# Optimization experiments

Measured on AMD Instinct MI355X. Metric: run time of the kernel, lower is better.

Reference implementation:

```python
import jax, jax.numpy as jnp
import numpy as np

B, T, C = 8, 2048, 1024
E = 8            # num_experts (= world_size in the original)
K = 2            # top-k
CAP_FACTOR = 1.25
CAPACITY = int(T / E * CAP_FACTOR)  # 320, per (expert, batch-row)
DFF = 4 * C


def setup_inputs() -> dict:
    key = jax.random.key(0)
    ks = jax.random.split(key, 4)
    x = jax.random.normal(ks[0], (B, T, C), dtype=jnp.float32)
    Wg = jax.random.normal(ks[1], (C, E), dtype=jnp.float32) * (C ** -0.5)
    bg = jnp.zeros((E,), dtype=jnp.float32)
    W1 = jax.random.normal(ks[2], (E, C, DFF), dtype=jnp.float32) * (C ** -0.5)
    b1 = jnp.zeros((E, DFF), dtype=jnp.float32)
    W2 = jax.random.normal(ks[3], (E, DFF, C), dtype=jnp.float32) * (DFF ** -0.5)
    b2 = jnp.zeros((E, C), dtype=jnp.float32)
    return {"x": x, "Wg": Wg, "bg": bg, "W1": W1, "b1": b1, "W2": W2, "b2": b2}


def reference(x, Wg, bg, W1, b1, W2, b2):
    # Router: linear + softmax, then top-k gating
    probs = jax.nn.softmax(jnp.einsum('btc,ce->bte', x, Wg) + bg, axis=-1)  # [B,T,E]
    topk_p, topk_e = jax.lax.top_k(probs, K)                               # [B,T,K]

    S = T * K  # one "assignment" per (token, k-slot), row-major (t, k) order
    e_flat = topk_e.reshape(B, S)                      # expert id per assignment
    p_flat = topk_p.reshape(B, S)

    # Position of each assignment within its (batch-row, expert) group,
    # ordered by token position then k-slot (matches nonzero() row-major order).
    onehot = (e_flat[..., None] == jnp.arange(E)).astype(jnp.int32)        # [B,S,E]
    pos_all = jnp.cumsum(onehot, axis=1) - 1                                # [B,S,E]
    pos = jnp.take_along_axis(pos_all, e_flat[..., None], axis=2)[..., 0]   # [B,S]
    keep = pos < CAPACITY                               # overflow tokens are dropped

    # Dispatch tokens into padded per-(expert,row) buffers: [E,B,CAPACITY,C]
    x_rep = jnp.repeat(x, K, axis=1)                    # [B,S,C], assignment order
    b_idx = jnp.broadcast_to(jnp.arange(B)[:, None], (B, S))
    pos_scat = jnp.where(keep, pos, CAPACITY)           # out-of-range -> dropped
    dispatch = jnp.zeros((E, B, CAPACITY, C), dtype=x.dtype)
    dispatch = dispatch.at[e_flat, b_idx, pos_scat].set(x_rep, mode='drop')

    # Grouped expert FFN (padding rows are zeros; their outputs are never read back)
    h = jax.nn.relu(jnp.einsum('ebsc,ech->ebsh', dispatch, W1) + b1[:, None, None, :])
    y = jnp.einsum('ebsh,ehc->ebsc', h, W2) + b2[:, None, None, :]

    # Combine: gather back, scale by gate prob (dropped tokens -> padding_val 0)
    gathered = y[e_flat, b_idx, jnp.clip(pos, 0, CAPACITY - 1)]             # [B,S,C]
    out = gathered * jnp.where(keep, p_flat, 0.0)[..., None]
    return out.reshape(B, T, K, C).sum(axis=2)          # sum over k assignments
```

## Files before the change

kernel.cpp:

```cpp
#include <hip/hip_runtime.h>
#include <stdint.h>

#define B_ 8
#define T_ 2048
#define C_ 1024
#define E_ 8
#define K_ 2
#define CAP_ 320
#define DFF_ 4096
#define S_ (T_*K_)
#define NTOK (B_*T_)
#define ROWS_PER_E (B_*CAP_)

typedef __attribute__((ext_vector_type(8))) short short8;
typedef __attribute__((ext_vector_type(4))) float floatx4;

__device__ __forceinline__ unsigned short f2bf(float f) {
  union { float f; unsigned u; } v; v.f = f;
  unsigned r = v.u + 0x7fffu + ((v.u >> 16) & 1u);
  return (unsigned short)(r >> 16);
}
__device__ __forceinline__ float bf2f(unsigned short h) {
  union { unsigned u; float f; } v; v.u = ((unsigned)h) << 16;
  return v.f;
}

#define GLOAD16(g, l) __builtin_amdgcn_global_load_lds( \
    (const __attribute__((address_space(1))) void*)(g), \
    (__attribute__((address_space(3))) void*)(l), 16, 0, 0)

__global__ void router_kernel(const float* __restrict__ x, const float* __restrict__ Wg,
                              const float* __restrict__ bg,
                              int* __restrict__ topk_e, float* __restrict__ topk_p)
{
  int token = (int)((blockIdx.x * blockDim.x + threadIdx.x) >> 6);
  int lane = threadIdx.x & 63;
  if (token >= NTOK) return;
  const float* xr = x + (size_t)token * C_;
  double acc[E_];
  #pragma unroll
  for (int e = 0; e < E_; ++e) acc[e] = 0.0;
  for (int c = lane; c < C_; c += 64) {
    double xv = (double)xr[c];
    const float4* w4 = (const float4*)(Wg + (size_t)c * E_);
    float4 wa = w4[0], wb = w4[1];
    acc[0] += xv * (double)wa.x; acc[1] += xv * (double)wa.y;
    acc[2] += xv * (double)wa.z; acc[3] += xv * (double)wa.w;
    acc[4] += xv * (double)wb.x; acc[5] += xv * (double)wb.y;
    acc[6] += xv * (double)wb.z; acc[7] += xv * (double)wb.w;
  }
  #pragma unroll
  for (int off = 32; off; off >>= 1) {
    #pragma unroll
    for (int e = 0; e < E_; ++e) acc[e] += __shfl_down(acc[e], off, 64);
  }
  if (lane == 0) {
    double lg[E_];
    double mx = -1e300;
    #pragma unroll
    for (int e = 0; e < E_; ++e) { lg[e] = acc[e] + (double)bg[e]; mx = fmax(mx, lg[e]); }
    double se = 0.0, pr[E_];
    #pragma unroll
    for (int e = 0; e < E_; ++e) { pr[e] = exp(lg[e] - mx); se += pr[e]; }
    #pragma unroll
    for (int e = 0; e < E_; ++e) pr[e] /= se;
    int e0 = 0;
    #pragma unroll
    for (int e = 1; e < E_; ++e) if (pr[e] > pr[e0]) e0 = e;
    int e1 = -1;
    #pragma unroll
    for (int e = 0; e < E_; ++e) {
      if (e == e0) continue;
      if (e1 < 0 || pr[e] > pr[e1]) e1 = e;
    }
    topk_e[token*2+0] = e0; topk_p[token*2+0] = (float)pr[e0];
    topk_e[token*2+1] = e1; topk_p[token*2+1] = (float)pr[e1];
  }
}

__global__ void scan_kernel(const int* __restrict__ topk_e,
                            int* __restrict__ pos_arr,
                            int* __restrict__ slot_src,
                            int* __restrict__ counts)
{
  const int b = blockIdx.x;
  const int tid = threadIdx.x;
  const int PT = S_ / 256;
  __shared__ int cnt[256][E_];
  int e_loc[16];
  int local[E_];
  #pragma unroll
  for (int e = 0; e < E_; ++e) local[e] = 0;
  const int* te = topk_e + (size_t)b * S_;
  for (int j = 0; j < PT; ++j) {
    int e = te[tid*PT + j];
    e_loc[j] = e;
    local[e]++;
  }
  #pragma unroll
  for (int e = 0; e < E_; ++e) cnt[tid][e] = local[e];
  __syncthreads();
  if (tid < E_) {
    int run = 0;
    for (int i = 0; i < 256; ++i) { int v = cnt[i][tid]; cnt[i][tid] = run; run += v; }
    counts[tid*B_ + b] = run;
  }
  __syncthreads();
  int base[E_];
  #pragma unroll
  for (int e = 0; e < E_; ++e) base[e] = cnt[tid][e];
  for (int j = 0; j < PT; ++j) {
    int e = e_loc[j];
    int p = base[e]++;
    int s = tid*PT + j;
    if (p < CAP_) {
      pos_arr[(size_t)b*S_ + s] = p;
      slot_src[((size_t)e*B_ + b)*CAP_ + p] = s >> 1;
    } else {
      pos_arr[(size_t)b*S_ + s] = -1;
    }
  }
}

__global__ void transpose_conv_kernel(const float* __restrict__ in, unsigned short* __restrict__ out,
                                      int R, int Cc)
{
  __shared__ float tile[32][33];
  const int e = blockIdx.z;
  const float* ine = in + (size_t)e * R * Cc;
  unsigned short* oute = out + (size_t)e * R * Cc;
  const int c0 = blockIdx.x * 32, r0 = blockIdx.y * 32;
  const int tx = threadIdx.x & 7, ty = threadIdx.x >> 3;
  float4 v = *(const float4*)(ine + (size_t)(r0 + ty) * Cc + c0 + tx*4);
  tile[ty][tx*4+0] = v.x; tile[ty][tx*4+1] = v.y;
  tile[ty][tx*4+2] = v.z; tile[ty][tx*4+3] = v.w;
  __syncthreads();
  ushort4 o;
  o.x = f2bf(tile[tx*4+0][ty]);
  o.y = f2bf(tile[tx*4+1][ty]);
  o.z = f2bf(tile[tx*4+2][ty]);
  o.w = f2bf(tile[tx*4+3][ty]);
  *(ushort4*)(oute + (size_t)(c0 + ty) * R + r0 + tx*4) = o;
}

__global__ void dispatch_kernel(const float* __restrict__ x, const int* __restrict__ slot_src,
                                const int* __restrict__ counts, unsigned short* __restrict__ Xd,
                                int e_base, int nexp)
{
  int row = (int)((blockIdx.x * blockDim.x + threadIdx.x) >> 6);
  int lane = threadIdx.x & 63;
  int total = nexp * B_ * CAP_;
  if (row >= total) return;
  int el = row / (B_*CAP_);
  int rem = row - el*(B_*CAP_);
  int b = rem / CAP_, slot = rem - b*CAP_;
  int eg = e_base + el;
  int cnt = counts[eg*B_ + b]; if (cnt > CAP_) cnt = CAP_;
  unsigned short* orow = Xd + (size_t)row * C_;
  if (slot < cnt) {
    int t = slot_src[((size_t)eg*B_ + b)*CAP_ + slot];
    const float4* xr = (const float4*)(x + ((size_t)b*T_ + t)*C_);
    #pragma unroll
    for (int i = 0; i < C_/256; ++i) {
      float4 v = xr[i*64 + lane];
      ushort4 o;
      o.x = f2bf(v.x); o.y = f2bf(v.y); o.z = f2bf(v.z); o.w = f2bf(v.w);
      ((ushort4*)orow)[i*64 + lane] = o;
    }
  } else {
    ushort4 z; z.x = z.y = z.z = z.w = 0;
    #pragma unroll
    for (int i = 0; i < C_/256; ++i) ((ushort4*)orow)[i*64 + lane] = z;
  }
}

template<int RELU>
__global__ __launch_bounds__(512) void gemm256_kernel(
    const unsigned short* __restrict__ A,
    const unsigned short* __restrict__ BT,
    const float* __restrict__ bias,
    unsigned short* __restrict__ Out0,
    unsigned short* __restrict__ Out1,
    int M, int N, int Kfull, int klen, int tilesPerSplit, int nwg)
{
  __shared__ __align__(16) unsigned short lds[4*16384];
  const int NT = N >> 8, MT = M >> 8;
  const int bid = blockIdx.x;
  const int wg = (bid & 7) * (nwg >> 3) + (bid >> 3);
  const int sp  = wg / tilesPerSplit;
  const int wgr = wg - sp * tilesPerSplit;
  const int e  = wgr / (MT*NT);
  const int r2 = wgr - e*(MT*NT);
  const int mt = r2 / NT, nt = r2 - mt*NT;
  const int k0 = sp * klen;
  const unsigned short* Ae = A + (size_t)e * M * Kfull;
  const unsigned short* Be = BT + (size_t)e * N * Kfull;
  const float* be = bias ? (bias + (size_t)e * N) : nullptr;
  unsigned short* Oe = (sp == 0 ? Out0 : Out1) + (size_t)e * M * N;
  const int m0 = mt*256, n0 = nt*256;

  const int tid = threadIdx.x, lane = tid & 63, w = tid >> 6;
  const int wr = w >> 2, wc = w & 3;

  floatx4 acc[8][4];
  #pragma unroll
  for (int i = 0; i < 8; ++i)
    #pragma unroll
    for (int j = 0; j < 4; ++j) acc[i][j] = (floatx4){0.f, 0.f, 0.f, 0.f};

  const int c0 = tid, c1 = 512 + tid;
  const int sr0 = c0 >> 2, sr1 = c1 >> 2;
  const int sq0 = ((c0 & 3) * 8) ^ (((sr0 >> 1) & 3) << 3);
  const int sq1 = ((c1 & 3) * 8) ^ (((sr1 >> 1) & 3) << 3);
  const unsigned short* gA0 = Ae + (size_t)(m0 + sr0)*Kfull + k0 + sq0;
  const unsigned short* gA1 = Ae + (size_t)(m0 + sr1)*Kfull + k0 + sq1;
  const unsigned short* gB0 = Be + (size_t)(n0 + sr0)*Kfull + k0 + sq0;
  const unsigned short* gB1 = Be + (size_t)(n0 + sr1)*Kfull + k0 + sq1;
  const int ldsOff0 = w*512;
  const int ldsOff1 = 4096 + w*512;

  const int fr = lane & 15, kq = lane >> 4;
  const int aRow = wr*128 + fr;
  const int bRow = wc*64 + fr;
  const int aOff = aRow*32 + ((kq*8) ^ (((aRow >> 1) & 3) << 3));
  const int bOff = 8192 + bRow*32 + ((kq*8) ^ (((bRow >> 1) & 3) << 3));

  const int nk = klen >> 5;

#define STAGE_A(t, slot) do { \
    GLOAD16(gA0 + (size_t)(t)*32, lds + (slot)*16384 + ldsOff0); \
    GLOAD16(gA1 + (size_t)(t)*32, lds + (slot)*16384 + ldsOff1); } while(0)
#define STAGE_B(t, slot) do { \
    GLOAD16(gB0 + (size_t)(t)*32, lds + (slot)*16384 + 8192 + ldsOff0); \
    GLOAD16(gB1 + (size_t)(t)*32, lds + (slot)*16384 + 8192 + ldsOff1); } while(0)

  STAGE_A(0, 0); STAGE_B(0, 0);
  STAGE_A(1, 1); STAGE_B(1, 1);
  STAGE_A(2, 2); STAGE_B(2, 2);
  asm volatile("s_waitcnt vmcnt(8)" ::: "memory");
  __builtin_amdgcn_s_barrier();

  for (int t = 0; t < nk; ++t) {
    const int slot = t & 3, ps = (t + 3) & 3;
    const unsigned short* sT = lds + slot*16384;
    const bool pf = (t + 3 < nk);
    short8 bfr[4], afLo[4], afHi[4];

    #pragma unroll
    for (int nf = 0; nf < 4; ++nf) bfr[nf] = *(const short8*)(sT + bOff + nf*512);
    #pragma unroll
    for (int mf = 0; mf < 4; ++mf) afLo[mf] = *(const short8*)(sT + aOff + mf*512);
    __builtin_amdgcn_sched_barrier(0);
    #pragma unroll
    for (int mf = 0; mf < 4; ++mf) afHi[mf] = *(const short8*)(sT + aOff + (mf+4)*512);
    if (pf) { STAGE_A(t+3, ps); STAGE_B(t+3, ps); }
    asm volatile("s_waitcnt lgkmcnt(4)" ::: "memory");
    __builtin_amdgcn_sched_barrier(0);
    __builtin_amdgcn_s_setprio(1);
    #pragma unroll
    for (int mf = 0; mf < 4; ++mf)
      #pragma unroll
      for (int nf = 0; nf < 4; ++nf)
        acc[mf][nf] = __builtin_amdgcn_mfma_f32_16x16x32_bf16(afLo[mf], bfr[nf], acc[mf][nf], 0, 0, 0);
    __builtin_amdgcn_s_setprio(0);
    __builtin_amdgcn_sched_barrier(0);
    asm volatile("s_waitcnt lgkmcnt(0)" ::: "memory");
    __builtin_amdgcn_sched_barrier(0);
    __builtin_amdgcn_s_setprio(1);
    #pragma unroll
    for (int mf = 0; mf < 4; ++mf)
      #pragma unroll
      for (int nf = 0; nf < 4; ++nf)
        acc[mf+4][nf] = __builtin_amdgcn_mfma_f32_16x16x32_bf16(afHi[mf], bfr[nf], acc[mf+4][nf], 0, 0, 0);
    __builtin_amdgcn_s_setprio(0);
    __builtin_amdgcn_sched_barrier(0);

    if (t + 1 < nk) {
      if (t + 3 < nk)      asm volatile("s_waitcnt vmcnt(8)" ::: "memory");
      else if (t + 2 < nk) asm volatile("s_waitcnt vmcnt(4)" ::: "memory");
      else                 asm volatile("s_waitcnt vmcnt(0)" ::: "memory");
      __builtin_amdgcn_s_barrier();
    }
  }
#undef STAGE_A
#undef STAGE_B

  const int col = lane & 15, rbase = (lane >> 4) * 4;
  #pragma unroll
  for (int mf = 0; mf < 8; ++mf) {
    const int gr0 = m0 + wr*128 + mf*16 + rbase;
    #pragma unroll
    for (int nf = 0; nf < 4; ++nf) {
      const int gc = n0 + wc*64 + nf*16 + col;
      const float bv = be ? be[gc] : 0.f;
      #pragma unroll
      for (int r = 0; r < 4; ++r) {
        float v = acc[mf][nf][r] + bv;
        if (RELU) v = fmaxf(v, 0.f);
        Oe[(size_t)(gr0 + r)*N + gc] = f2bf(v);
      }
    }
  }
}

__global__ void combine_kernel(const unsigned short* __restrict__ Y0,
                               const unsigned short* __restrict__ Y1,
                               const float* __restrict__ b2c,
                               const int* __restrict__ topk_e, const float* __restrict__ topk_p,
                               const int* __restrict__ pos_arr, float* __restrict__ out)
{
  int token = (int)((blockIdx.x * blockDim.x + threadIdx.x) >> 6);
  int lane = threadIdx.x & 63;
  if (token >= NTOK) return;
  int b = token / T_, t = token - b*T_;
  int s0 = b*S_ + t*2;
  float acc[16];
  #pragma unroll
  for (int i = 0; i < 16; ++i) acc[i] = 0.f;
  #pragma unroll
  for (int k = 0; k < 2; ++k) {
    int pos = pos_arr[s0 + k];
    if (pos < 0) continue;
    int e = topk_e[s0 + k];
    float p = topk_p[s0 + k];
    size_t rowoff = (((size_t)e*B_ + b)*CAP_ + pos) * C_;
    const unsigned short* yr0 = Y0 + rowoff;
    const unsigned short* yr1 = Y1 ? (Y1 + rowoff) : nullptr;
    const float* bb = b2c ? (b2c + (size_t)e * C_) : nullptr;
    #pragma unroll
    for (int i = 0; i < 4; ++i) {
      ushort4 v = ((const ushort4*)yr0)[i*64 + lane];
      float s0v = bf2f(v.x), s1v = bf2f(v.y), s2v = bf2f(v.z), s3v = bf2f(v.w);
      if (yr1) {
        ushort4 u = ((const ushort4*)yr1)[i*64 + lane];
        s0v += bf2f(u.x); s1v += bf2f(u.y); s2v += bf2f(u.z); s3v += bf2f(u.w);
      }
      if (bb) {
        float4 bv = ((const float4*)bb)[i*64 + lane];
        s0v += bv.x; s1v += bv.y; s2v += bv.z; s3v += bv.w;
      }
      acc[i*4+0] += p * s0v;
      acc[i*4+1] += p * s1v;
      acc[i*4+2] += p * s2v;
      acc[i*4+3] += p * s3v;
    }
  }
  float4* orow = (float4*)(out + (size_t)token * C_);
  #pragma unroll
  for (int i = 0; i < 4; ++i) {
    float4 o;
    o.x = acc[i*4+0]; o.y = acc[i*4+1]; o.z = acc[i*4+2]; o.w = acc[i*4+3];
    orow[i*64 + lane] = o;
  }
}

extern "C" void kernel_launch(void* const* d_in, const int* in_sizes, int n_in,
                              void* d_out, int out_size, void* d_ws, size_t ws_size,
                              hipStream_t stream)
{
  const float* x  = (const float*)d_in[0];
  const float* Wg = (const float*)d_in[1];
  const float* bg = (const float*)d_in[2];
  const float* W1 = (const float*)d_in[3];
  const float* b1 = (const float*)d_in[4];
  const float* W2 = (const float*)d_in[5];
  const float* b2 = (const float*)d_in[6];
  float* out = (float*)d_out;

  char* ws = (char*)d_ws;
  size_t off = 0;
  auto alloc = [&](size_t bytes) -> char* {
    char* p = ws + off;
    off = (off + bytes + 255) & ~(size_t)255;
    return p;
  };
  int*   topk_e  = (int*)  alloc((size_t)NTOK * K_ * 4);
  float* topk_p  = (float*)alloc((size_t)NTOK * K_ * 4);
  int*   pos_arr = (int*)  alloc((size_t)B_ * S_ * 4);
  int*   slot_src= (int*)  alloc((size_t)E_ * B_ * CAP_ * 4);
  int*   counts  = (int*)  alloc((size_t)E_ * B_ * 4);
  unsigned short* Ybuf = (unsigned short*)alloc((size_t)E_ * ROWS_PER_E * C_ * 2);
  size_t fixed = off;
  const size_t perE = (size_t)C_ * DFF_ * 2
                    + (size_t)ROWS_PER_E * C_ * 2
                    + (size_t)ROWS_PER_E * DFF_ * 2
                    + 3 * 256;
  int k = 8;
  while (k > 1 && fixed + (size_t)k * perE > ws_size) k >>= 1;
  unsigned short* Wt = (unsigned short*)alloc((size_t)k * C_ * DFF_ * 2);
  unsigned short* Xd = (unsigned short*)alloc((size_t)k * ROWS_PER_E * C_ * 2);
  unsigned short* Hb = (unsigned short*)alloc((size_t)k * ROWS_PER_E * DFF_ * 2);

  router_kernel<<<NTOK/4, 256, 0, stream>>>(x, Wg, bg, topk_e, topk_p);
  scan_kernel<<<B_, 256, 0, stream>>>(topk_e, pos_arr, slot_src, counts);

  const bool splitK2 = (k == 8);

  for (int eb = 0; eb < E_; eb += k) {
    transpose_conv_kernel<<<dim3(DFF_/32, C_/32, k), 256, 0, stream>>>(
        W1 + (size_t)eb * C_ * DFF_, Wt, C_, DFF_);
    dispatch_kernel<<<(k * ROWS_PER_E) / 4, 256, 0, stream>>>(x, slot_src, counts, Xd, eb, k);
    {
      int tiles = k * (ROWS_PER_E/256) * (DFF_/256);
      gemm256_kernel<1><<<tiles, 512, 0, stream>>>(
          Xd, Wt, b1 + (size_t)eb * DFF_, Hb, Hb, ROWS_PER_E, DFF_, C_, C_, tiles, tiles);
    }
    transpose_conv_kernel<<<dim3(C_/32, DFF_/32, k), 256, 0, stream>>>(
        W2 + (size_t)eb * DFF_ * C_, Wt, DFF_, C_);
    {
      int tiles = k * (ROWS_PER_E/256) * (C_/256);
      if (splitK2) {
        gemm256_kernel<0><<<2*tiles, 512, 0, stream>>>(
            Hb, Wt, nullptr, Ybuf, Xd, ROWS_PER_E, C_, DFF_, DFF_/2, tiles, 2*tiles);
      } else {
        gemm256_kernel<0><<<tiles, 512, 0, stream>>>(
            Hb, Wt, b2 + (size_t)eb * C_, Ybuf + (size_t)eb * ROWS_PER_E * C_,
            Ybuf + (size_t)eb * ROWS_PER_E * C_, ROWS_PER_E, C_, DFF_, DFF_, tiles, tiles);
      }
    }
  }

  combine_kernel<<<NTOK/4, 256, 0, stream>>>(
      Ybuf, splitK2 ? Xd : nullptr, splitK2 ? b2 : nullptr,
      topk_e, topk_p, pos_arr, out);
}
```

Baseline: 589.4 us.

## Switch expert GEMMs to 256x128 tiles with 4 waves and 3-stage pipeline

```diff
diff --git a/kernel.cpp b/kernel.cpp
--- a/kernel.cpp
+++ b/kernel.cpp
@@ -175,7 +175,7 @@
 }
 
 template<int RELU>
-__global__ __launch_bounds__(512) void gemm256_kernel(
+__global__ __launch_bounds__(256, 2) void gemm256x128_kernel(
     const unsigned short* __restrict__ A,
     const unsigned short* __restrict__ BT,
     const float* __restrict__ bias,
@@ -183,8 +183,8 @@
     unsigned short* __restrict__ Out1,
     int M, int N, int Kfull, int klen, int tilesPerSplit, int nwg)
 {
-  __shared__ __align__(16) unsigned short lds[4*16384];
-  const int NT = N >> 8, MT = M >> 8;
+  __shared__ __align__(16) unsigned short lds[3*12288];
+  const int NT = N >> 7, MT = M >> 8;
   const int bid = blockIdx.x;
   const int wg = (bid & 7) * (nwg >> 3) + (bid >> 3);
   const int sp  = wg / tilesPerSplit;
@@ -197,10 +197,10 @@
   const unsigned short* Be = BT + (size_t)e * N * Kfull;
   const float* be = bias ? (bias + (size_t)e * N) : nullptr;
   unsigned short* Oe = (sp == 0 ? Out0 : Out1) + (size_t)e * M * N;
-  const int m0 = mt*256, n0 = nt*256;
+  const int m0 = mt*256, n0 = nt*128;
 
   const int tid = threadIdx.x, lane = tid & 63, w = tid >> 6;
-  const int wr = w >> 2, wc = w & 3;
+  const int wr = w >> 1, wc = w & 1;
 
   floatx4 acc[8][4];
   #pragma unroll
@@ -208,16 +208,20 @@
     #pragma unroll
     for (int j = 0; j < 4; ++j) acc[i][j] = (floatx4){0.f, 0.f, 0.f, 0.f};
 
-  const int c0 = tid, c1 = 512 + tid;
-  const int sr0 = c0 >> 2, sr1 = c1 >> 2;
-  const int sq0 = ((c0 & 3) * 8) ^ (((sr0 >> 1) & 3) << 3);
-  const int sq1 = ((c1 & 3) * 8) ^ (((sr1 >> 1) & 3) << 3);
-  const unsigned short* gA0 = Ae + (size_t)(m0 + sr0)*Kfull + k0 + sq0;
-  const unsigned short* gA1 = Ae + (size_t)(m0 + sr1)*Kfull + k0 + sq1;
-  const unsigned short* gB0 = Be + (size_t)(n0 + sr0)*Kfull + k0 + sq0;
-  const unsigned short* gB1 = Be + (size_t)(n0 + sr1)*Kfull + k0 + sq1;
-  const int ldsOff0 = w*512;
-  const int ldsOff1 = 4096 + w*512;
+  const int ca0 = tid, ca1 = 256 + tid, ca2 = 512 + tid, ca3 = 768 + tid;
+  const int ra0 = ca0 >> 2, ra1 = ca1 >> 2, ra2 = ca2 >> 2, ra3 = ca3 >> 2;
+  const int qa0 = ((ca0 & 3)*8) ^ (((ra0 >> 1) & 3) << 3);
+  const int qa1 = ((ca1 & 3)*8) ^ (((ra1 >> 1) & 3) << 3);
+  const int qa2 = ((ca2 & 3)*8) ^ (((ra2 >> 1) & 3) << 3);
+  const int qa3 = ((ca3 & 3)*8) ^ (((ra3 >> 1) & 3) << 3);
+  const unsigned short* gA0 = Ae + (size_t)(m0 + ra0)*Kfull + k0 + qa0;
+  const unsigned short* gA1 = Ae + (size_t)(m0 + ra1)*Kfull + k0 + qa1;
+  const unsigned short* gA2 = Ae + (size_t)(m0 + ra2)*Kfull + k0 + qa2;
+  const unsigned short* gA3 = Ae + (size_t)(m0 + ra3)*Kfull + k0 + qa3;
+  const unsigned short* gB0 = Be + (size_t)(n0 + ra0)*Kfull + k0 + qa0;
+  const unsigned short* gB1 = Be + (size_t)(n0 + ra1)*Kfull + k0 + qa1;
+  const int la0 = w*512, la1 = 2048 + w*512, la2 = 4096 + w*512, la3 = 6144 + w*512;
+  const int lb0 = 8192 + w*512, lb1 = 8192 + 2048 + w*512;
 
   const int fr = lane & 15, kq = lane >> 4;
   const int aRow = wr*128 + fr;
@@ -227,23 +231,23 @@
 
   const int nk = klen >> 5;
 
-#define STAGE_A(t, slot) do { \
-    GLOAD16(gA0 + (size_t)(t)*32, lds + (slot)*16384 + ldsOff0); \
-    GLOAD16(gA1 + (size_t)(t)*32, lds + (slot)*16384 + ldsOff1); } while(0)
-#define STAGE_B(t, slot) do { \
-    GLOAD16(gB0 + (size_t)(t)*32, lds + (slot)*16384 + 8192 + ldsOff0); \
-    GLOAD16(gB1 + (size_t)(t)*32, lds + (slot)*16384 + 8192 + ldsOff1); } while(0)
-
-  STAGE_A(0, 0); STAGE_B(0, 0);
-  STAGE_A(1, 1); STAGE_B(1, 1);
-  STAGE_A(2, 2); STAGE_B(2, 2);
-  asm volatile("s_waitcnt vmcnt(8)" ::: "memory");
+#define STAGE(t, slot) do { \
+    GLOAD16(gA0 + (size_t)(t)*32, lds + (slot)*12288 + la0); \
+    GLOAD16(gA1 + (size_t)(t)*32, lds + (slot)*12288 + la1); \
+    GLOAD16(gA2 + (size_t)(t)*32, lds + (slot)*12288 + la2); \
+    GLOAD16(gA3 + (size_t)(t)*32, lds + (slot)*12288 + la3); \
+    GLOAD16(gB0 + (size_t)(t)*32, lds + (slot)*12288 + lb0); \
+    GLOAD16(gB1 + (size_t)(t)*32, lds + (slot)*12288 + lb1); } while(0)
+
+  STAGE(0, 0); STAGE(1, 1);
+  asm volatile("s_waitcnt vmcnt(6)" ::: "memory");
   __builtin_amdgcn_s_barrier();
 
   for (int t = 0; t < nk; ++t) {
-    const int slot = t & 3, ps = (t + 3) & 3;
-    const unsigned short* sT = lds + slot*16384;
-    const bool pf = (t + 3 < nk);
+    const int slot  = t % 3;
+    const int ps    = (t + 2) % 3;
+    const unsigned short* sT = lds + slot*12288;
+    const bool pf = (t + 2 < nk);
     short8 bfr[4], afLo[4], afHi[4];
 
     #pragma unroll
@@ -253,7 +257,7 @@
     __builtin_amdgcn_sched_barrier(0);
     #pragma unroll
     for (int mf = 0; mf < 4; ++mf) afHi[mf] = *(const short8*)(sT + aOff + (mf+4)*512);
-    if (pf) { STAGE_A(t+3, ps); STAGE_B(t+3, ps); }
+    if (pf) STAGE(t+2, ps);
     asm volatile("s_waitcnt lgkmcnt(4)" ::: "memory");
     __builtin_amdgcn_sched_barrier(0);
     __builtin_amdgcn_s_setprio(1);
@@ -276,14 +280,12 @@
     __builtin_amdgcn_sched_barrier(0);
 
     if (t + 1 < nk) {
-      if (t + 3 < nk)      asm volatile("s_waitcnt vmcnt(8)" ::: "memory");
-      else if (t + 2 < nk) asm volatile("s_waitcnt vmcnt(4)" ::: "memory");
-      else                 asm volatile("s_waitcnt vmcnt(0)" ::: "memory");
+      if (t + 2 < nk) asm volatile("s_waitcnt vmcnt(6)" ::: "memory");
+      else            asm volatile("s_waitcnt vmcnt(0)" ::: "memory");
       __builtin_amdgcn_s_barrier();
     }
   }
-#undef STAGE_A
-#undef STAGE_B
+#undef STAGE
 
   const int col = lane & 15, rbase = (lane >> 4) * 4;
   #pragma unroll
@@ -401,19 +403,19 @@
         W1 + (size_t)eb * C_ * DFF_, Wt, C_, DFF_);
     dispatch_kernel<<<(k * ROWS_PER_E) / 4, 256, 0, stream>>>(x, slot_src, counts, Xd, eb, k);
     {
-      int tiles = k * (ROWS_PER_E/256) * (DFF_/256);
-      gemm256_kernel<1><<<tiles, 512, 0, stream>>>(
+      int tiles = k * (ROWS_PER_E/256) * (DFF_/128);
+      gemm256x128_kernel<1><<<tiles, 256, 0, stream>>>(
           Xd, Wt, b1 + (size_t)eb * DFF_, Hb, Hb, ROWS_PER_E, DFF_, C_, C_, tiles, tiles);
     }
     transpose_conv_kernel<<<dim3(C_/32, DFF_/32, k), 256, 0, stream>>>(
         W2 + (size_t)eb * DFF_ * C_, Wt, DFF_, C_);
     {
-      int tiles = k * (ROWS_PER_E/256) * (C_/256);
+      int tiles = k * (ROWS_PER_E/256) * (C_/128);
       if (splitK2) {
-        gemm256_kernel<0><<<2*tiles, 512, 0, stream>>>(
+        gemm256x128_kernel<0><<<2*tiles, 256, 0, stream>>>(
             Hb, Wt, nullptr, Ybuf, Xd, ROWS_PER_E, C_, DFF_, DFF_/2, tiles, 2*tiles);
       } else {
-        gemm256_kernel<0><<<tiles, 512, 0, stream>>>(
+        gemm256x128_kernel<0><<<tiles, 256, 0, stream>>>(
             Hb, Wt, b2 + (size_t)eb * C_, Ybuf + (size_t)eb * ROWS_PER_E * C_,
             Ybuf + (size_t)eb * ROWS_PER_E * C_, ROWS_PER_E, C_, DFF_, DFF_, tiles, tiles);
       }
```

Measured after the change: 593.4 us. About the same (+0.7%).

## Shrink GEMM tiles to 128x128 with triple-buffered LDS and widen transpose stores

Applied to the files above, without the earlier changes.

```diff
diff --git a/kernel.cpp b/kernel.cpp
--- a/kernel.cpp
+++ b/kernel.cpp
@@ -125,22 +125,24 @@
 __global__ void transpose_conv_kernel(const float* __restrict__ in, unsigned short* __restrict__ out,
                                       int R, int Cc)
 {
-  __shared__ float tile[32][33];
+  __shared__ float tile[64][33];
   const int e = blockIdx.z;
   const float* ine = in + (size_t)e * R * Cc;
   unsigned short* oute = out + (size_t)e * R * Cc;
-  const int c0 = blockIdx.x * 32, r0 = blockIdx.y * 32;
+  const int c0 = blockIdx.x * 32, r0 = blockIdx.y * 64;
   const int tx = threadIdx.x & 7, ty = threadIdx.x >> 3;
-  float4 v = *(const float4*)(ine + (size_t)(r0 + ty) * Cc + c0 + tx*4);
-  tile[ty][tx*4+0] = v.x; tile[ty][tx*4+1] = v.y;
-  tile[ty][tx*4+2] = v.z; tile[ty][tx*4+3] = v.w;
+  #pragma unroll
+  for (int p = 0; p < 2; ++p) {
+    const int rr = p*32 + ty;
+    float4 v = *(const float4*)(ine + (size_t)(r0 + rr) * Cc + c0 + tx*4);
+    tile[rr][tx*4+0] = v.x; tile[rr][tx*4+1] = v.y;
+    tile[rr][tx*4+2] = v.z; tile[rr][tx*4+3] = v.w;
+  }
   __syncthreads();
-  ushort4 o;
-  o.x = f2bf(tile[tx*4+0][ty]);
-  o.y = f2bf(tile[tx*4+1][ty]);
-  o.z = f2bf(tile[tx*4+2][ty]);
-  o.w = f2bf(tile[tx*4+3][ty]);
-  *(ushort4*)(oute + (size_t)(c0 + ty) * R + r0 + tx*4) = o;
+  short8 s;
+  #pragma unroll
+  for (int j = 0; j < 8; ++j) s[j] = (short)f2bf(tile[tx*8+j][ty]);
+  *(short8*)(oute + (size_t)(c0 + ty) * R + r0 + tx*8) = s;
 }
 
 __global__ void dispatch_kernel(const float* __restrict__ x, const int* __restrict__ slot_src,
@@ -175,7 +177,7 @@
 }
 
 template<int RELU>
-__global__ __launch_bounds__(512) void gemm256_kernel(
+__global__ __launch_bounds__(256, 3) void gemm128_kernel(
     const unsigned short* __restrict__ A,
     const unsigned short* __restrict__ BT,
     const float* __restrict__ bias,
@@ -183,8 +185,8 @@
     unsigned short* __restrict__ Out1,
     int M, int N, int Kfull, int klen, int tilesPerSplit, int nwg)
 {
-  __shared__ __align__(16) unsigned short lds[4*16384];
-  const int NT = N >> 8, MT = M >> 8;
+  __shared__ __align__(16) unsigned short lds[3*8192];
+  const int NT = N >> 7, MT = M >> 7;
   const int bid = blockIdx.x;
   const int wg = (bid & 7) * (nwg >> 3) + (bid >> 3);
   const int sp  = wg / tilesPerSplit;
@@ -197,98 +199,77 @@
   const unsigned short* Be = BT + (size_t)e * N * Kfull;
   const float* be = bias ? (bias + (size_t)e * N) : nullptr;
   unsigned short* Oe = (sp == 0 ? Out0 : Out1) + (size_t)e * M * N;
-  const int m0 = mt*256, n0 = nt*256;
+  const int m0 = mt*128, n0 = nt*128;
 
   const int tid = threadIdx.x, lane = tid & 63, w = tid >> 6;
-  const int wr = w >> 2, wc = w & 3;
-
-  floatx4 acc[8][4];
-  #pragma unroll
-  for (int i = 0; i < 8; ++i)
+  const int wr = w >> 1, wc = w & 1;
+
+  floatx4 acc[4][4];
+  #pragma unroll
+  for (int i = 0; i < 4; ++i)
     #pragma unroll
     for (int j = 0; j < 4; ++j) acc[i][j] = (floatx4){0.f, 0.f, 0.f, 0.f};
 
-  const int c0 = tid, c1 = 512 + tid;
+  const int c0 = tid, c1 = 256 + tid;
   const int sr0 = c0 >> 2, sr1 = c1 >> 2;
-  const int sq0 = ((c0 & 3) * 8) ^ (((sr0 >> 1) & 3) << 3);
-  const int sq1 = ((c1 & 3) * 8) ^ (((sr1 >> 1) & 3) << 3);
+  const int sq0 = ((c0 & 3)*8) ^ (((sr0 >> 1) & 3) << 3);
+  const int sq1 = ((c1 & 3)*8) ^ (((sr1 >> 1) & 3) << 3);
   const unsigned short* gA0 = Ae + (size_t)(m0 + sr0)*Kfull + k0 + sq0;
   const unsigned short* gA1 = Ae + (size_t)(m0 + sr1)*Kfull + k0 + sq1;
   const unsigned short* gB0 = Be + (size_t)(n0 + sr0)*Kfull + k0 + sq0;
   const unsigned short* gB1 = Be + (size_t)(n0 + sr1)*Kfull + k0 + sq1;
-  const int ldsOff0 = w*512;
-  const int ldsOff1 = 4096 + w*512;
+  const int la0 = w*512, la1 = 2048 + w*512;
+  const int lb0 = 4096 + w*512, lb1 = 4096 + 2048 + w*512;
 
   const int fr = lane & 15, kq = lane >> 4;
-  const int aRow = wr*128 + fr;
+  const int aRow = wr*64 + fr;
   const int bRow = wc*64 + fr;
   const int aOff = aRow*32 + ((kq*8) ^ (((aRow >> 1) & 3) << 3));
-  const int bOff = 8192 + bRow*32 + ((kq*8) ^ (((bRow >> 1) & 3) << 3));
+  const int bOff = 4096 + bRow*32 + ((kq*8) ^ (((bRow >> 1) & 3) << 3));
 
   const int nk = klen >> 5;
 
-#define STAGE_A(t, slot) do { \
-    GLOAD16(gA0 + (size_t)(t)*32, lds + (slot)*16384 + ldsOff0); \
-    GLOAD16(gA1 + (size_t)(t)*32, lds + (slot)*16384 + ldsOff1); } while(0)
-#define STAGE_B(t, slot) do { \
-    GLOAD16(gB0 + (size_t)(t)*32, lds + (slot)*16384 + 8192 + ldsOff0); \
-    GLOAD16(gB1 + (size_t)(t)*32, lds + (slot)*16384 + 8192 + ldsOff1); } while(0)
-
-  STAGE_A(0, 0); STAGE_B(0, 0);
-  STAGE_A(1, 1); STAGE_B(1, 1);
-  STAGE_A(2, 2); STAGE_B(2, 2);
-  asm volatile("s_waitcnt vmcnt(8)" ::: "memory");
+#define STAGE(t, slot) do { \
+    GLOAD16(gA0 + (size_t)(t)*32, lds + (slot)*8192 + la0); \
+    GLOAD16(gA1 + (size_t)(t)*32, lds + (slot)*8192 + la1); \
+    GLOAD16(gB0 + (size_t)(t)*32, lds + (slot)*8192 + lb0); \
+    GLOAD16(gB1 + (size_t)(t)*32, lds + (slot)*8192 + lb1); } while(0)
+
+  STAGE(0, 0); STAGE(1, 1);
+  asm volatile("s_waitcnt vmcnt(4)" ::: "memory");
   __builtin_amdgcn_s_barrier();
 
   for (int t = 0; t < nk; ++t) {
-    const int slot = t & 3, ps = (t + 3) & 3;
-    const unsigned short* sT = lds + slot*16384;
-    const bool pf = (t + 3 < nk);
-    short8 bfr[4], afLo[4], afHi[4];
-
-    #pragma unroll
-    for (int nf = 0; nf < 4; ++nf) bfr[nf] = *(const short8*)(sT + bOff + nf*512);
-    #pragma unroll
-    for (int mf = 0; mf < 4; ++mf) afLo[mf] = *(const short8*)(sT + aOff + mf*512);
-    __builtin_amdgcn_sched_barrier(0);
-    #pragma unroll
-    for (int mf = 0; mf < 4; ++mf) afHi[mf] = *(const short8*)(sT + aOff + (mf+4)*512);
-    if (pf) { STAGE_A(t+3, ps); STAGE_B(t+3, ps); }
-    asm volatile("s_waitcnt lgkmcnt(4)" ::: "memory");
-    __builtin_amdgcn_sched_barrier(0);
-    __builtin_amdgcn_s_setprio(1);
+    const int slot = t % 3;
+    const int ps   = (t + 2) % 3;
+    const unsigned short* sT = lds + slot*8192;
+
+    short8 af[4], bf[4];
+    #pragma unroll
+    for (int mf = 0; mf < 4; ++mf) af[mf] = *(const short8*)(sT + aOff + mf*512);
+    #pragma unroll
+    for (int nf = 0; nf < 4; ++nf) bf[nf] = *(const short8*)(sT + bOff + nf*512);
+    if (t + 2 < nk) STAGE(t+2, ps);
+
     #pragma unroll
     for (int mf = 0; mf < 4; ++mf)
       #pragma unroll
       for (int nf = 0; nf < 4; ++nf)
-        acc[mf][nf] = __builtin_amdgcn_mfma_f32_16x16x32_bf16(afLo[mf], bfr[nf], acc[mf][nf], 0, 0, 0);
-    __builtin_amdgcn_s_setprio(0);
-    __builtin_amdgcn_sched_barrier(0);
-    asm volatile("s_waitcnt lgkmcnt(0)" ::: "memory");
-    __builtin_amdgcn_sched_barrier(0);
-    __builtin_amdgcn_s_setprio(1);
-    #pragma unroll
-    for (int mf = 0; mf < 4; ++mf)
-      #pragma unroll
-      for (int nf = 0; nf < 4; ++nf)
-        acc[mf+4][nf] = __builtin_amdgcn_mfma_f32_16x16x32_bf16(afHi[mf], bfr[nf], acc[mf+4][nf], 0, 0, 0);
-    __builtin_amdgcn_s_setprio(0);
-    __builtin_amdgcn_sched_barrier(0);
+        acc[mf][nf] = __builtin_amdgcn_mfma_f32_16x16x32_bf16(af[mf], bf[nf], acc[mf][nf], 0, 0, 0);
 
     if (t + 1 < nk) {
-      if (t + 3 < nk)      asm volatile("s_waitcnt vmcnt(8)" ::: "memory");
-      else if (t + 2 < nk) asm volatile("s_waitcnt vmcnt(4)" ::: "memory");
-      else                 asm volatile("s_waitcnt vmcnt(0)" ::: "memory");
+      asm volatile("s_waitcnt lgkmcnt(0)" ::: "memory");
+      if (t + 2 < nk) asm volatile("s_waitcnt vmcnt(4)" ::: "memory");
+      else            asm volatile("s_waitcnt vmcnt(0)" ::: "memory");
       __builtin_amdgcn_s_barrier();
     }
   }
-#undef STAGE_A
-#undef STAGE_B
+#undef STAGE
 
   const int col = lane & 15, rbase = (lane >> 4) * 4;
   #pragma unroll
-  for (int mf = 0; mf < 8; ++mf) {
-    const int gr0 = m0 + wr*128 + mf*16 + rbase;
+  for (int mf = 0; mf < 4; ++mf) {
+    const int gr0 = m0 + wr*64 + mf*16 + rbase;
     #pragma unroll
     for (int nf = 0; nf < 4; ++nf) {
       const int gc = n0 + wc*64 + nf*16 + col;
@@ -397,23 +378,23 @@
   const bool splitK2 = (k == 8);
 
   for (int eb = 0; eb < E_; eb += k) {
-    transpose_conv_kernel<<<dim3(DFF_/32, C_/32, k), 256, 0, stream>>>(
+    transpose_conv_kernel<<<dim3(DFF_/32, C_/64, k), 256, 0, stream>>>(
         W1 + (size_t)eb * C_ * DFF_, Wt, C_, DFF_);
     dispatch_kernel<<<(k * ROWS_PER_E) / 4, 256, 0, stream>>>(x, slot_src, counts, Xd, eb, k);
     {
-      int tiles = k * (ROWS_PER_E/256) * (DFF_/256);
-      gemm256_kernel<1><<<tiles, 512, 0, stream>>>(
+      int tiles = k * (ROWS_PER_E/128) * (DFF_/128);
+      gemm128_kernel<1><<<tiles, 256, 0, stream>>>(
           Xd, Wt, b1 + (size_t)eb * DFF_, Hb, Hb, ROWS_PER_E, DFF_, C_, C_, tiles, tiles);
     }
-    transpose_conv_kernel<<<dim3(C_/32, DFF_/32, k), 256, 0, stream>>>(
+    transpose_conv_kernel<<<dim3(C_/32, DFF_/64, k), 256, 0, stream>>>(
         W2 + (size_t)eb * DFF_ * C_, Wt, DFF_, C_);
     {
-      int tiles = k * (ROWS_PER_E/256) * (C_/256);
+      int tiles = k * (ROWS_PER_E/128) * (C_/128);
       if (splitK2) {
-        gemm256_kernel<0><<<2*tiles, 512, 0, stream>>>(
+        gemm128_kernel<0><<<2*tiles, 256, 0, stream>>>(
             Hb, Wt, nullptr, Ybuf, Xd, ROWS_PER_E, C_, DFF_, DFF_/2, tiles, 2*tiles);
       } else {
-        gemm256_kernel<0><<<tiles, 512, 0, stream>>>(
+        gemm128_kernel<0><<<tiles, 256, 0, stream>>>(
             Hb, Wt, b2 + (size_t)eb * C_, Ybuf + (size_t)eb * ROWS_PER_E * C_,
             Ybuf + (size_t)eb * ROWS_PER_E * C_, ROWS_PER_E, C_, DFF_, DFF_, tiles, tiles);
       }
```

After: 630.6 us. 1.07x slower.
